# Kernel optimization log

Hardware: AMD Instinct MI355X
Metric: run time of the kernel (lower is better)

Reference implementation:

```python
import jax, jax.numpy as jnp
import numpy as np

B, S, D, H, F, L, V, SPAN = 4, 1024, 1024, 16, 4096, 4, 32000, 512
DH = D // H
NEG = -1e9


def _ln(x, g, b, eps=1e-12):
    m = x.mean(-1, keepdims=True)
    v = ((x - m) ** 2).mean(-1, keepdims=True)
    return (x - m) * jax.lax.rsqrt(v + eps) * g + b


def setup_inputs() -> dict:
    key = jax.random.key(0)
    ks = iter(jax.random.split(key, 40))
    g = lambda shape: jax.random.normal(next(ks), shape, jnp.float32) * 0.02
    inp = {
        "input_ids": jax.random.randint(next(ks), (B, S), 0, V),
        "segment_ids": jnp.zeros((B, S), jnp.int32),
        "attention_mask": jnp.ones((B, S), jnp.float32),
        "tok_emb": g((V, D)),
        "seg_emb": g((2, D)),
        "emb_ln_g": jnp.ones((D,), jnp.float32),
        "emb_ln_b": jnp.zeros((D,), jnp.float32),
        "rel_emb": g((2 * SPAN, D)),
        "Wq": g((L, D, D)), "bq": jnp.zeros((L, D), jnp.float32),
        "Wk": g((L, D, D)), "bk": jnp.zeros((L, D), jnp.float32),
        "Wv": g((L, D, D)), "bv": jnp.zeros((L, D), jnp.float32),
        "Wo": g((L, D, D)), "bo": jnp.zeros((L, D), jnp.float32),
        "ln1_g": jnp.ones((L, D), jnp.float32), "ln1_b": jnp.zeros((L, D), jnp.float32),
        "W1": g((L, D, F)), "b1": jnp.zeros((L, F), jnp.float32),
        "W2": g((L, F, D)), "b2": jnp.zeros((L, D), jnp.float32),
        "ln2_g": jnp.ones((L, D), jnp.float32), "ln2_b": jnp.zeros((L, D), jnp.float32),
    }
    return inp


def _forward(input_ids, segment_ids, attention_mask, tok_emb, seg_emb, emb_ln_g,
             emb_ln_b, rel_emb, Wq, bq, Wk, bk, Wv, bv, Wo, bo, ln1_g, ln1_b,
             W1, b1, W2, b2, ln2_g, ln2_b):
    # BertEmbedding (max_len=0 => no absolute positions): token + segment, LN, mask
    h = _ln(tok_emb[input_ids] + seg_emb[segment_ids], emb_ln_g, emb_ln_b)
    h = h * attention_mask[..., None]

    # relative positions (bucket_size=0 path): rel[q,k] = q - k, clamped into table
    pos = jnp.arange(S)
    rel = pos[:, None] - pos[None, :]                      # [S,S]
    c2p_idx = jnp.clip(rel + SPAN, 0, 2 * SPAN - 1)        # [S,S]
    p2c_idx = jnp.clip(-rel + SPAN, 0, 2 * SPAN - 1)       # [S,S]
    bias = (1.0 - attention_mask)[:, None, None, :] * NEG  # [B,1,1,S] additive mask

    scale = 1.0 / jnp.sqrt(jnp.asarray(DH * 3, h.dtype))   # scale_factor = 1 + |{c2p,p2c}|

    def layer(h, p):
        wq, bq_, wk, bk_, wv, bv_, wo, bo_, g1, b1n, w1, b1f, w2, b2f, g2, b2n = p
        q = (h @ wq + bq_).reshape(B, S, H, DH)
        k = (h @ wk + bk_).reshape(B, S, H, DH)
        v = (h @ wv + bv_).reshape(B, S, H, DH)
        att = jnp.einsum('bqhd,bkhd->bhqk', q, k) * scale
        # disentangled relative-position bias (shared q/k projections on rel table)
        pos_k = (rel_emb @ wk + bk_).reshape(2 * SPAN, H, DH)
        pos_q = (rel_emb @ wq + bq_).reshape(2 * SPAN, H, DH)
        c2p = jnp.einsum('bqhd,phd->bhqp', q, pos_k) * scale   # [B,H,S,2*SPAN]
        att = att + jnp.take_along_axis(c2p, c2p_idx[None, None], axis=-1)
        p2c = jnp.einsum('bkhd,phd->bhkp', k, pos_q) * scale   # [B,H,S,2*SPAN]
        att = att + jnp.swapaxes(
            jnp.take_along_axis(p2c, p2c_idx[None, None], axis=-1), -1, -2)
        probs = jax.nn.softmax(att + bias, axis=-1)
        ctx = jnp.einsum('bhqk,bkhd->bqhd', probs, v).reshape(B, S, D)
        h = _ln(h + ctx @ wo + bo_, g1, b1n)
        ff = jax.nn.gelu(h @ w1 + b1f, approximate=False) @ w2 + b2f
        return _ln(h + ff, g2, b2n), None

    h, _ = jax.lax.scan(layer, h, (Wq, bq, Wk, bk, Wv, bv, Wo, bo,
                                   ln1_g, ln1_b, W1, b1, W2, b2, ln2_g, ln2_b))
    return h


def reference(input_ids, segment_ids, attention_mask, tok_emb, seg_emb, emb_ln_g,
              emb_ln_b, rel_emb, Wq, bq, Wk, bk, Wv, bv, Wo, bo, ln1_g, ln1_b,
              W1, b1, W2, b2, ln2_g, ln2_b):
    return _forward(input_ids, segment_ids, attention_mask, tok_emb, seg_emb,
                    emb_ln_g, emb_ln_b, rel_emb, Wq, bq, Wk, bk, Wv, bv, Wo, bo,
                    ln1_g, ln1_b, W1, b1, W2, b2, ln2_g, ln2_b)
```

## Files before the change

kernel.cpp:

```cpp
#include <hip/hip_runtime.h>

#define DEV __device__ __forceinline__

typedef __bf16 bf16;
typedef __bf16 bf16x4 __attribute__((ext_vector_type(4)));
typedef __bf16 bf16x8 __attribute__((ext_vector_type(8)));
typedef float f32x4 __attribute__((ext_vector_type(4)));

constexpr int B_ = 4, S_ = 1024, D_ = 1024, H_ = 16, F_ = 4096, L_ = 4, SPAN_ = 512, DH_ = 64;
constexpr float SCALE_ = 0.07216878364870322f;
constexpr float LOG2E_ = 1.4426950408889634f;
constexpr float SCL2_ = SCALE_ * LOG2E_;
constexpr float THR2_ = 11.5f;
constexpr long POSL_ = 32L * 1024 * 64;

DEV void gload_lds16(const void* g, void* l) {
  __builtin_amdgcn_global_load_lds((const __attribute__((address_space(1))) void*)g,
                                   (__attribute__((address_space(3))) void*)l, 16, 0, 0);
}

template <int CTRL>
DEV float dppf(float x) {
  return __builtin_bit_cast(
      float, __builtin_amdgcn_mov_dpp(__builtin_bit_cast(int, x), CTRL, 0xf, 0xf, true));
}
DEV float rowMax16(float v) {
  v = fmaxf(v, dppf<0x128>(v));
  v = fmaxf(v, dppf<0x124>(v));
  v = fmaxf(v, dppf<0x122>(v));
  v = fmaxf(v, dppf<0x121>(v));
  return v;
}
DEV float rowSum16(float v) {
  v += dppf<0x128>(v);
  v += dppf<0x124>(v);
  v += dppf<0x122>(v);
  v += dppf<0x121>(v);
  return v;
}

DEV float blockSum4(float v, volatile float* red) {
#pragma unroll
  for (int o = 32; o; o >>= 1) v += __shfl_xor(v, o);
  if ((threadIdx.x & 63) == 0) red[threadIdx.x >> 6] = v;
  __syncthreads();
  return red[0] + red[1] + red[2] + red[3];
}

DEV bf16x8 lds_frag(const bf16* buf, int row, int chunk) {
  return *(const bf16x8*)((const char*)buf + row * 128 + ((chunk ^ (row & 7)) << 4));
}
DEV bf16x8 rdfrag(const char* base, int row, int chunk) {
  return *(const bf16x8*)(base + row * 128 + ((chunk ^ (row & 7)) << 4));
}

template <int EPI>
__global__ __launch_bounds__(512, 1) void gemm256(
    const bf16* __restrict__ A, const bf16* __restrict__ Bm,
    const float* __restrict__ bias, void* __restrict__ Cout,
    int K, int lda, int ldb, int ldc, long sA, long sB, long sC) {
  extern __shared__ __align__(16) char smem[];

  const int z = blockIdx.z;
  A += (long)z * sA;
  Bm += (long)z * sB;
  const long coff = (long)z * sC;

  const int nwg = gridDim.x * gridDim.y;
  const int flat = blockIdx.y * gridDim.x + blockIdx.x;
  const int qq = nwg >> 3;
  const int swz = (flat & 7) * qq + (flat >> 3);
  const int bx = swz % gridDim.x, by = swz / gridDim.x;
  const int m0 = by * 256, n0 = bx * 256;

  const int tid = threadIdx.x, lane = tid & 63, wave = tid >> 6;
  const int wr = wave >> 2, wc = wave & 3;
  const int fr = lane & 15, fq = lane >> 4;

  f32x4 acc[8][4];
#pragma unroll
  for (int m = 0; m < 8; m++)
#pragma unroll
    for (int n = 0; n < 4; n++) acc[m][n] = f32x4{0.f, 0.f, 0.f, 0.f};

  const int r8 = tid >> 3;
  const int swzel = ((tid & 7) ^ (r8 & 7)) << 3;
  const bf16* ga = A + (long)(m0 + r8) * lda + swzel;
  const bf16* gb = Bm + (long)(n0 + r8) * ldb + swzel;

  const int NT = K >> 6;

  auto stage = [&](int t) {
    const long ko = (long)t * 64;
    char* da = smem + ((t & 1) << 15) + wave * 1024;
    gload_lds16(ga + ko, da);
    gload_lds16(ga + 64 * (long)lda + ko, da + 8192);
    gload_lds16(ga + 128 * (long)lda + ko, da + 16384);
    gload_lds16(ga + 192 * (long)lda + ko, da + 24576);
    char* db = smem + 65536 + ((t & 1) << 15) + wave * 1024;
    gload_lds16(gb + ko, db);
    gload_lds16(gb + 64 * (long)ldb + ko, db + 8192);
    gload_lds16(gb + 128 * (long)ldb + ko, db + 16384);
    gload_lds16(gb + 192 * (long)ldb + ko, db + 24576);
  };

  stage(0);
  asm volatile("s_waitcnt vmcnt(0)" ::: "memory");
  __builtin_amdgcn_s_barrier();

  for (int j = 0; j < NT; j++) {
    const char* Ac = smem + ((j & 1) << 15);
    const char* Bc = smem + 65536 + ((j & 1) << 15);

    if (j + 1 < NT) stage(j + 1);

    bf16x8 af[4][2], bfg[4][2];
#pragma unroll
    for (int m = 0; m < 4; m++) {
      const int ar = wr * 128 + m * 16 + fr;
      af[m][0] = rdfrag(Ac, ar, fq);
      af[m][1] = rdfrag(Ac, ar, 4 + fq);
    }
#pragma unroll
    for (int n = 0; n < 4; n++) {
      const int br = wc * 64 + n * 16 + fr;
      bfg[n][0] = rdfrag(Bc, br, fq);
      bfg[n][1] = rdfrag(Bc, br, 4 + fq);
    }

    __builtin_amdgcn_s_setprio(1);
#pragma unroll
    for (int m = 0; m < 4; m++)
#pragma unroll
      for (int n = 0; n < 4; n++)
#pragma unroll
        for (int kc = 0; kc < 2; kc++)
          acc[m][n] = __builtin_amdgcn_mfma_f32_16x16x32_bf16(af[m][kc], bfg[n][kc],
                                                              acc[m][n], 0, 0, 0);
    __builtin_amdgcn_s_setprio(0);
    __builtin_amdgcn_sched_barrier(0);

#pragma unroll
    for (int m = 0; m < 4; m++) {
      const int ar = wr * 128 + (m + 4) * 16 + fr;
      af[m][0] = rdfrag(Ac, ar, fq);
      af[m][1] = rdfrag(Ac, ar, 4 + fq);
    }
    __builtin_amdgcn_s_setprio(1);
#pragma unroll
    for (int m = 0; m < 4; m++)
#pragma unroll
      for (int n = 0; n < 4; n++)
#pragma unroll
        for (int kc = 0; kc < 2; kc++)
          acc[m + 4][n] = __builtin_amdgcn_mfma_f32_16x16x32_bf16(af[m][kc], bfg[n][kc],
                                                                  acc[m + 4][n], 0, 0, 0);
    __builtin_amdgcn_s_setprio(0);

    asm volatile("s_waitcnt vmcnt(0)" ::: "memory");
    __builtin_amdgcn_s_barrier();
  }

#pragma unroll
  for (int m = 0; m < 8; m++) {
#pragma unroll
    for (int n = 0; n < 4; n++) {
      const int col = n0 + wc * 64 + n * 16 + fr;
      float bval = 0.f;
      if constexpr (EPI == 3 || EPI == 4) bval = bias ? bias[col] : 0.f;
#pragma unroll
      for (int rr = 0; rr < 4; rr++) {
        const int row = m0 + wr * 128 + m * 16 + fq * 4 + rr;
        const long idx = coff + (long)row * ldc + col;
        const float v = acc[m][n][rr];
        if constexpr (EPI == 0) ((float*)Cout)[idx] = v;
        else if constexpr (EPI == 3) ((bf16*)Cout)[idx] = (bf16)(v + bval);
        else if constexpr (EPI == 4) {
          float x = v + bval;
          x = 0.5f * x * (1.f + erff(x * 0.70710678118654752f));
          ((bf16*)Cout)[idx] = (bf16)x;
        }
      }
    }
  }
}

template <int EPI>
__global__ __launch_bounds__(256) void gemm_bt(
    const bf16* __restrict__ A, const bf16* __restrict__ Bm,
    const float* __restrict__ bias, void* __restrict__ Cout,
    int M, int N, int K, int lda, int ldb, int ldc, float alpha,
    long sA, long sB, long sC, long sBias) {
  __shared__ alignas(16) bf16 As[128 * 64];
  __shared__ alignas(16) bf16 Bs[128 * 64];

  const int z = blockIdx.z;
  A += (long)z * sA;
  Bm += (long)z * sB;
  bias += (long)z * sBias;
  const long coff = (long)z * sC;

  const int nwg = gridDim.x * gridDim.y;
  const int flat = blockIdx.y * gridDim.x + blockIdx.x;
  const int qq = nwg >> 3;
  const int swz = (flat & 7) * qq + (flat >> 3);
  const int bx = swz % gridDim.x, by = swz / gridDim.x;

  const int m0 = by * 128, n0 = bx * 128;
  const int tid = threadIdx.x, lane = tid & 63, wave = tid >> 6;
  const int wr = wave >> 1, wc = wave & 1;
  const int fr = lane & 15, fq = lane >> 4;

  f32x4 acc[4][4];
#pragma unroll
  for (int m = 0; m < 4; m++)
#pragma unroll
    for (int n = 0; n < 4; n++) acc[m][n] = f32x4{0.f, 0.f, 0.f, 0.f};

  const int r8 = tid >> 3;
  const int swzel = ((tid & 7) ^ (r8 & 7)) << 3;
  const bf16* ga = A + (long)(m0 + r8) * lda + swzel;
  const bf16* gb = Bm + (long)(n0 + r8) * ldb + swzel;
  const int swzrd = fr & 7;

  for (int k0 = 0; k0 < K; k0 += 64) {
#pragma unroll
    for (int i = 0; i < 4; i++)
      gload_lds16(ga + (long)i * 32 * lda + k0, (char*)As + i * 4096 + wave * 1024);
#pragma unroll
    for (int i = 0; i < 4; i++)
      gload_lds16(gb + (long)i * 32 * ldb + k0, (char*)Bs + i * 4096 + wave * 1024);
    __syncthreads();
#pragma unroll
    for (int kc = 0; kc < 2; kc++) {
      bf16x8 af[4], bfv[4];
#pragma unroll
      for (int m = 0; m < 4; m++)
        af[m] = *(const bf16x8*)((char*)As + (wr * 64 + m * 16 + fr) * 128 +
                                 (((kc * 4 + fq) ^ swzrd) << 4));
#pragma unroll
      for (int n = 0; n < 4; n++)
        bfv[n] = *(const bf16x8*)((char*)Bs + (wc * 64 + n * 16 + fr) * 128 +
                                  (((kc * 4 + fq) ^ swzrd) << 4));
#pragma unroll
      for (int m = 0; m < 4; m++)
#pragma unroll
        for (int n = 0; n < 4; n++)
          acc[m][n] = __builtin_amdgcn_mfma_f32_16x16x32_bf16(af[m], bfv[n], acc[m][n], 0, 0, 0);
    }
    __syncthreads();
  }

#pragma unroll
  for (int m = 0; m < 4; m++) {
#pragma unroll
    for (int n = 0; n < 4; n++) {
      const int col = n0 + wc * 64 + n * 16 + fr;
      float bval = 0.f;
      if constexpr (EPI == 3 || EPI == 4 || EPI == 5) bval = bias ? bias[col] : 0.f;
#pragma unroll
      for (int rr = 0; rr < 4; rr++) {
        const int row = m0 + wr * 64 + m * 16 + fq * 4 + rr;
        const long idx = coff + (long)row * ldc + col;
        const float v = acc[m][n][rr];
        if constexpr (EPI == 0) ((float*)Cout)[idx] = v * alpha;
        else if constexpr (EPI == 3) ((bf16*)Cout)[idx] = (bf16)(v + bval);
        else if constexpr (EPI == 4) {
          float x = v + bval;
          x = 0.5f * x * (1.f + erff(x * 0.70710678118654752f));
          ((bf16*)Cout)[idx] = (bf16)x;
        } else if constexpr (EPI == 5) {
          const long pidx = coff + ((long)(col >> 6) * 1024 + row) * 64 + (col & 63);
          ((bf16*)Cout)[pidx] = (bf16)(v + bval);
        }
      }
    }
  }
}

__global__ __launch_bounds__(256) void repack_kv(const bf16* __restrict__ qkv,
                                                 bf16* __restrict__ kp,
                                                 bf16* __restrict__ vp) {
  const int kt = blockIdx.x, bh = blockIdx.y;
  const int b = bh >> 4, h = bh & 15;
  const int k0 = kt * 64;
  __shared__ bf16 t[64][72];
  const int ty = threadIdx.x >> 3, tx = threadIdx.x & 7;
#pragma unroll
  for (int p = 0; p < 2; p++) {
    const int s = k0 + p * 32 + ty;
    const long base = (long)(b * 1024 + s) * 3072 + h * 64;
    bf16x8 kv = *(const bf16x8*)(qkv + base + 1024 + tx * 8);
    *(bf16x8*)(kp + ((long)(bh * 1024 + s) << 6) + tx * 8) = kv;
    bf16x8 vv = *(const bf16x8*)(qkv + base + 2048 + tx * 8);
    *(bf16x8*)(&t[p * 32 + ty][tx * 8]) = vv;
  }
  __syncthreads();
  const int dh = threadIdx.x >> 2, sc = (threadIdx.x & 3) * 16;
  bf16 tmp[16];
#pragma unroll
  for (int j = 0; j < 16; j++) tmp[j] = t[sc + j][dh];
  bf16* dst = vp + ((long)(bh * 16 + kt) << 12) + dh * 64 + sc;
  *(bf16x8*)dst = *(bf16x8*)tmp;
  *(bf16x8*)(dst + 8) = *(bf16x8*)(tmp + 8);
}

__global__ __launch_bounds__(256) void attn_fused(
    const bf16* __restrict__ qkv, const bf16* __restrict__ kp,
    const bf16* __restrict__ vp, const bf16* __restrict__ pospk,
    const float* __restrict__ mask, bf16* __restrict__ ctx) {
  const int id = blockIdx.x;
  const int xcd = id & 7, sub = id >> 3;
  const int bh = xcd + 8 * (sub >> 4);
  const int qt = sub & 15;
  const int b = bh >> 4, h = bh & 15;
  const int q0 = qt * 64;
  const int tid = threadIdx.x, wave = tid >> 6, lane = tid & 63;
  const int fr = lane & 15, fq = lane >> 4;

  __shared__ alignas(16) char smem[79360];
  bf16* PXk = (bf16*)smem;
  char* p_l = smem;
  bf16* PXq = (bf16*)(smem + 16384);
  bf16* Ks = (bf16*)(smem + 32768);
  bf16* Vs = (bf16*)(smem + 40960);
  bf16* c2p_T = (bf16*)(smem + 49152);
  bf16* p2c_T = (bf16*)(smem + 61952);

  const bf16* posq = pospk + ((long)h << 16);
  const bf16* posk = pospk + ((long)(16 + h) << 16);
  const bf16* kbase = kp + ((long)bh << 16);
  const bf16* vbase = vp + ((long)bh << 16);

  bf16x8 qa[2];
  {
    const bf16* qrow = qkv + (long)(b * 1024 + q0 + wave * 16 + fr) * 3072 + h * 64;
    qa[0] = *(const bf16x8*)(qrow + fq * 8);
    qa[1] = *(const bf16x8*)(qrow + 32 + fq * 8);
  }

  f32x4 o[4];
#pragma unroll
  for (int n = 0; n < 4; n++) o[n] = f32x4{0.f, 0.f, 0.f, 0.f};
  float m_r[4], l_r[4];
#pragma unroll
  for (int r = 0; r < 4; r++) { m_r[r] = -1e30f; l_r[r] = 0.f; }

  char* pl_base = p_l + wave * 2048;
  bf16* c2p_w = c2p_T + wave * 1600;
  const int wbyte = wave * 1024;

  for (int kt = 0; kt < 16; kt++) {
    const int k0 = kt * 64;

    __syncthreads();
    {
      const int j0k = q0 - k0 + 449;
      const int j0q = k0 - q0 + 449;
#pragma unroll
      for (int c = 0; c < 4; c++) {
        const int u = c * 256 + tid;
        const int rr = u >> 3;
        const int sel = (((u & 7) ^ (rr & 7)) << 3);
        int jk = j0k + rr;
        jk = jk < 0 ? 0 : (jk > 1023 ? 1023 : jk);
        gload_lds16(posk + ((long)jk << 6) + sel, (char*)PXk + c * 4096 + wbyte);
        int jq = j0q + rr;
        jq = jq < 0 ? 0 : (jq > 1023 ? 1023 : jq);
        gload_lds16(posq + ((long)jq << 6) + sel, (char*)PXq + c * 4096 + wbyte);
      }
#pragma unroll
      for (int c = 0; c < 2; c++) {
        const int u = c * 256 + tid;
        const int rr = u >> 3;
        const int sel = (((u & 7) ^ (rr & 7)) << 3);
        gload_lds16(kbase + ((long)(k0 + rr) << 6) + sel, (char*)Ks + c * 4096 + wbyte);
        gload_lds16(vbase + ((long)kt << 12) + ((long)rr << 6) + sel,
                    (char*)Vs + c * 4096 + wbyte);
      }
    }
    __syncthreads();

    bf16x8 ka[2];
    ka[0] = lds_frag(Ks, wave * 16 + fr, fq);
    ka[1] = lds_frag(Ks, wave * 16 + fr, 4 + fq);
    __builtin_amdgcn_s_setprio(1);
    {
      f32x4 cw[5];
#pragma unroll
      for (int t = 0; t < 5; t++) cw[t] = f32x4{0.f, 0.f, 0.f, 0.f};
#pragma unroll
      for (int kc = 0; kc < 2; kc++)
#pragma unroll
        for (int t = 0; t < 5; t++) {
          const bf16x8 pb = lds_frag(PXk, wave * 16 + t * 16 + fr, kc * 4 + fq);
          cw[t] = __builtin_amdgcn_mfma_f32_16x16x32_bf16(qa[kc], pb, cw[t], 0, 0, 0);
        }
#pragma unroll
      for (int t = 0; t < 5; t++) {
        bf16x4 pk;
#pragma unroll
        for (int r = 0; r < 4; r++) pk[r] = (bf16)cw[t][r];
        *(bf16x4*)&c2p_w[(t * 16 + fr) * 20 + fq * 4] = pk;
      }
    }
    f32x4 s[4];
#pragma unroll
    for (int n = 0; n < 4; n++) s[n] = f32x4{0.f, 0.f, 0.f, 0.f};
#pragma unroll
    for (int kc = 0; kc < 2; kc++)
#pragma unroll
      for (int n = 0; n < 4; n++) {
        const bf16x8 kb = lds_frag(Ks, n * 16 + fr, kc * 4 + fq);
        s[n] = __builtin_amdgcn_mfma_f32_16x16x32_bf16(qa[kc], kb, s[n], 0, 0, 0);
      }
    {
      f32x4 pw[5];
#pragma unroll
      for (int t = 0; t < 5; t++) pw[t] = f32x4{0.f, 0.f, 0.f, 0.f};
#pragma unroll
      for (int kc = 0; kc < 2; kc++)
#pragma unroll
        for (int t = 0; t < 5; t++) {
          const bf16x8 pb = lds_frag(PXq, (wave + t) * 16 + fr, kc * 4 + fq);
          pw[t] = __builtin_amdgcn_mfma_f32_16x16x32_bf16(ka[kc], pb, pw[t], 0, 0, 0);
        }
#pragma unroll
      for (int t = 0; t < 5; t++) {
        bf16x4 pk;
#pragma unroll
        for (int r = 0; r < 4; r++) pk[r] = (bf16)pw[t][r];
        *(bf16x4*)&p2c_T[((wave + t) * 16 + fr) * 68 + wave * 16 + fq * 4] = pk;
      }
    }
    __builtin_amdgcn_s_setprio(0);
    __syncthreads();

    bf16x8 vb[2][4];
#pragma unroll
    for (int kc = 0; kc < 2; kc++)
#pragma unroll
      for (int n = 0; n < 4; n++) vb[kc][n] = lds_frag(Vs, n * 16 + fr, kc * 4 + fq);

    float st[4][4];
#pragma unroll
    for (int n = 0; n < 4; n++) {
      const int ki = n * 16 + fr;
      const float mb = (1.0f - mask[b * S_ + k0 + ki]) * (-1e9f * LOG2E_);
#pragma unroll
      for (int r = 0; r < 4; r++) {
        const int qi_s = fq * 4 + r;
        const float cv = (float)c2p_w[(qi_s - ki + 63) * 20 + qi_s];
        const float pv = (float)p2c_T[(ki - (wave * 16 + qi_s) + 63) * 68 + ki];
        st[n][r] = (s[n][r] + cv + pv) * SCL2_ + mb;
      }
    }

    float pmax[4];
#pragma unroll
    for (int r = 0; r < 4; r++) {
      float v = fmaxf(fmaxf(st[0][r], st[1][r]), fmaxf(st[2][r], st[3][r]));
      pmax[r] = rowMax16(v);
    }
    const bool ok = (pmax[0] - m_r[0] <= THR2_) && (pmax[1] - m_r[1] <= THR2_) &&
                    (pmax[2] - m_r[2] <= THR2_) && (pmax[3] - m_r[3] <= THR2_);
    if (!__all(ok)) {
#pragma unroll
      for (int r = 0; r < 4; r++) {
        const float mn = fmaxf(m_r[r], pmax[r]);
        const float sc = exp2f(m_r[r] - mn);
        m_r[r] = mn;
        l_r[r] *= sc;
#pragma unroll
        for (int n = 0; n < 4; n++) o[n][r] *= sc;
      }
    }
    float rs[4] = {0.f, 0.f, 0.f, 0.f};
#pragma unroll
    for (int n = 0; n < 4; n++) {
      const int ki = n * 16 + fr;
#pragma unroll
      for (int r = 0; r < 4; r++) {
        const int qi_s = fq * 4 + r;
        const float p = exp2f(st[n][r] - m_r[r]);
        rs[r] += p;
        *(bf16*)(pl_base + qi_s * 128 + ((ki * 2) ^ ((qi_s & 7) << 4))) = (bf16)p;
      }
    }
#pragma unroll
    for (int r = 0; r < 4; r++) l_r[r] += rowSum16(rs[r]);

#pragma unroll
    for (int kc = 0; kc < 2; kc++) {
      const bf16x8 pa =
          *(const bf16x8*)(pl_base + fr * 128 + ((kc * 64 + fq * 16) ^ ((fr & 7) << 4)));
#pragma unroll
      for (int n = 0; n < 4; n++)
        o[n] = __builtin_amdgcn_mfma_f32_16x16x32_bf16(pa, vb[kc][n], o[n], 0, 0, 0);
    }
  }

#pragma unroll
  for (int r = 0; r < 4; r++) {
    const float inv = 1.f / l_r[r];
    const long row = (long)(b * S_ + q0 + wave * 16 + fq * 4 + r) * D_ + h * 64;
#pragma unroll
    for (int n = 0; n < 4; n++) ctx[row + n * 16 + fr] = (bf16)(o[n][r] * inv);
  }
}

__global__ __launch_bounds__(256) void wtrans4(const float* __restrict__ Wq,
                                               const float* __restrict__ Wk,
                                               const float* __restrict__ Wv,
                                               const float* __restrict__ Wo,
                                               bf16* __restrict__ wqkvT,
                                               bf16* __restrict__ woT) {
  const int z = blockIdx.z;
  const int l = z >> 2, which = z & 3;
  const long DD = (long)D_ * D_;
  const float* W = (which == 0 ? Wq : which == 1 ? Wk : which == 2 ? Wv : Wo) + l * DD;
  bf16* WT = (which < 3) ? (wqkvT + (long)l * 3 * DD + which * DD) : (woT + (long)l * DD);
  __shared__ float t[32][33];
  const int n0 = blockIdx.x * 32, k0 = blockIdx.y * 32;
  const int tx = threadIdx.x & 31, ty = threadIdx.x >> 5;
#pragma unroll
  for (int i = ty; i < 32; i += 8) t[i][tx] = W[(long)(k0 + i) * D_ + n0 + tx];
  __syncthreads();
#pragma unroll
  for (int i = ty; i < 32; i += 8) WT[(long)(n0 + i) * D_ + k0 + tx] = (bf16)t[tx][i];
}

__global__ __launch_bounds__(256) void wtrans(const float* __restrict__ W,
                                              bf16* __restrict__ WT, int K, int N,
                                              long sW, long sT) {
  W += (long)blockIdx.z * sW;
  WT += (long)blockIdx.z * sT;
  __shared__ float t[32][33];
  const int n0 = blockIdx.x * 32, k0 = blockIdx.y * 32;
  const int tx = threadIdx.x & 31, ty = threadIdx.x >> 5;
#pragma unroll
  for (int i = ty; i < 32; i += 8) t[i][tx] = W[(long)(k0 + i) * N + n0 + tx];
  __syncthreads();
#pragma unroll
  for (int i = ty; i < 32; i += 8) WT[(long)(n0 + i) * K + k0 + tx] = (bf16)t[tx][i];
}

__global__ __launch_bounds__(256) void f2b(const float* __restrict__ in,
                                           bf16* __restrict__ out, long n) {
  long i = (long)blockIdx.x * 256 + threadIdx.x;
  if (i < n) out[i] = (bf16)in[i];
}

__global__ __launch_bounds__(256) void bias_concat(const float* __restrict__ bq,
                                                   const float* __restrict__ bk,
                                                   const float* __restrict__ bv,
                                                   float* __restrict__ bqkv) {
  const int i = blockIdx.x * 256 + threadIdx.x;
  const int l = i / (3 * D_), s = (i % (3 * D_)) / D_, d = i % D_;
  const float* src = s == 0 ? bq : (s == 1 ? bk : bv);
  bqkv[i] = src[l * D_ + d];
}

__global__ __launch_bounds__(256) void embed_ln(
    const int* __restrict__ ids, const int* __restrict__ segs,
    const float* __restrict__ mask, const float* __restrict__ tok,
    const float* __restrict__ seg, const float* __restrict__ g,
    const float* __restrict__ bta, float* __restrict__ h, bf16* __restrict__ hb) {
  __shared__ float r1[4], r2[4];
  const int t = blockIdx.x;
  const int d4 = threadIdx.x;
  const long tb4 = (long)ids[t] * 256;
  const long sb4 = (long)segs[t] * 256;
  const long b4 = (long)t * 256;
  f32x4 x = ((const f32x4*)tok)[tb4 + d4];
  const f32x4 sv = ((const f32x4*)seg)[sb4 + d4];
#pragma unroll
  for (int r = 0; r < 4; r++) x[r] += sv[r];
  float sm = x[0] + x[1] + x[2] + x[3];
  sm = blockSum4(sm, r1);
  const float mean = sm * (1.f / D_);
  float vs = 0.f;
#pragma unroll
  for (int r = 0; r < 4; r++) {
    const float c = x[r] - mean;
    vs += c * c;
  }
  vs = blockSum4(vs, r2);
  const float rstd = rsqrtf(vs * (1.f / D_) + 1e-12f);
  const float mk = mask[t];
  const f32x4 gv = ((const f32x4*)g)[d4];
  const f32x4 bv = ((const f32x4*)bta)[d4];
  f32x4 y;
  bf16x4 yb;
#pragma unroll
  for (int r = 0; r < 4; r++) {
    y[r] = ((x[r] - mean) * rstd * gv[r] + bv[r]) * mk;
    yb[r] = (bf16)y[r];
  }
  ((f32x4*)h)[b4 + d4] = y;
  *(bf16x4*)&hb[(b4 + d4) * 4] = yb;
}

template <int P>
__global__ __launch_bounds__(256) void ln_residual_red(
    const float* __restrict__ hin, float* __restrict__ hout,
    const float* __restrict__ part, long pstride4,
    const float* __restrict__ bias, const float* __restrict__ g,
    const float* __restrict__ bta, bf16* __restrict__ hb) {
  __shared__ float r1[4], r2[4];
  const int d4 = threadIdx.x;
  const long b4 = (long)blockIdx.x * 256;
  f32x4 x = ((const f32x4*)hin)[b4 + d4];
  const f32x4 bi = ((const f32x4*)bias)[d4];
#pragma unroll
  for (int r = 0; r < 4; r++) x[r] += bi[r];
#pragma unroll
  for (int z = 0; z < P; z++) {
    const f32x4 pv = ((const f32x4*)part)[(long)z * pstride4 + b4 + d4];
#pragma unroll
    for (int r = 0; r < 4; r++) x[r] += pv[r];
  }
  float sm = x[0] + x[1] + x[2] + x[3];
  sm = blockSum4(sm, r1);
  const float mean = sm * (1.f / D_);
  float vs = 0.f;
#pragma unroll
  for (int r = 0; r < 4; r++) {
    const float c = x[r] - mean;
    vs += c * c;
  }
  vs = blockSum4(vs, r2);
  const float rstd = rsqrtf(vs * (1.f / D_) + 1e-12f);
  const f32x4 gv = ((const f32x4*)g)[d4];
  const f32x4 bv = ((const f32x4*)bta)[d4];
  f32x4 y;
  bf16x4 yb;
#pragma unroll
  for (int r = 0; r < 4; r++) {
    y[r] = (x[r] - mean) * rstd * gv[r] + bv[r];
    yb[r] = (bf16)y[r];
  }
  ((f32x4*)hout)[b4 + d4] = y;
  *(bf16x4*)&hb[(b4 + d4) * 4] = yb;
}

extern "C" void kernel_launch(void* const* d_in, const int* in_sizes, int n_in,
                              void* d_out, int out_size, void* d_ws, size_t ws_size,
                              hipStream_t stream) {
  (void)in_sizes; (void)n_in; (void)out_size; (void)ws_size;
  const int* input_ids = (const int*)d_in[0];
  const int* segment_ids = (const int*)d_in[1];
  const float* attention_mask = (const float*)d_in[2];
  const float* tok_emb = (const float*)d_in[3];
  const float* seg_emb = (const float*)d_in[4];
  const float* emb_ln_g = (const float*)d_in[5];
  const float* emb_ln_b = (const float*)d_in[6];
  const float* rel_emb = (const float*)d_in[7];
  const float* Wq = (const float*)d_in[8];
  const float* bq = (const float*)d_in[9];
  const float* Wk = (const float*)d_in[10];
  const float* bk = (const float*)d_in[11];
  const float* Wv = (const float*)d_in[12];
  const float* bv = (const float*)d_in[13];
  const float* Wo = (const float*)d_in[14];
  const float* bo = (const float*)d_in[15];
  const float* ln1_g = (const float*)d_in[16];
  const float* ln1_b = (const float*)d_in[17];
  const float* W1 = (const float*)d_in[18];
  const float* b1 = (const float*)d_in[19];
  const float* W2 = (const float*)d_in[20];
  const float* b2 = (const float*)d_in[21];
  const float* ln2_g = (const float*)d_in[22];
  const float* ln2_b = (const float*)d_in[23];

  const long DD = (long)D_ * D_;
  const long DF = (long)D_ * F_;
  const int D3 = 3 * D_;

  char* ws = (char*)d_ws;
  auto alloc = [&](size_t bytes) {
    char* p = ws;
    ws += (bytes + 255) & ~(size_t)255;
    return p;
  };
  bf16* wqkvT = (bf16*)alloc((size_t)L_ * 3 * DD * 2);
  bf16* woT = (bf16*)alloc((size_t)L_ * DD * 2);
  bf16* w1T = (bf16*)alloc((size_t)L_ * DF * 2);
  bf16* w2T = (bf16*)alloc((size_t)L_ * DF * 2);
  float* bqkv = (float*)alloc((size_t)L_ * 3 * D_ * 4);
  bf16* relb = (bf16*)alloc((size_t)2 * SPAN_ * D_ * 2);
  float* hbuf = (float*)alloc((size_t)B_ * S_ * D_ * 4);
  bf16* hb = (bf16*)alloc((size_t)B_ * S_ * D_ * 2);
  bf16* qkv = (bf16*)alloc((size_t)B_ * S_ * 3 * D_ * 2);
  bf16* kp = (bf16*)alloc((size_t)B_ * H_ * S_ * DH_ * 2);
  bf16* vp = (bf16*)alloc((size_t)B_ * H_ * S_ * DH_ * 2);
  bf16* pospk = (bf16*)alloc((size_t)L_ * POSL_ * 2);
  bf16* ctxb = (bf16*)alloc((size_t)B_ * S_ * D_ * 2);
  bf16* ff1b = (bf16*)alloc((size_t)B_ * S_ * F_ * 2);
  float* kpart = (float*)alloc((size_t)4 * B_ * S_ * D_ * 4);
  const long PSTR = (long)B_ * S_ * D_;

  wtrans4<<<dim3(D_ / 32, D_ / 32, 4 * L_), 256, 0, stream>>>(Wq, Wk, Wv, Wo, wqkvT, woT);
  wtrans<<<dim3(F_ / 32, D_ / 32, L_), 256, 0, stream>>>(W1, w1T, D_, F_, DF, DF);
  wtrans<<<dim3(D_ / 32, F_ / 32, L_), 256, 0, stream>>>(W2, w2T, F_, D_, DF, DF);
  bias_concat<<<dim3(L_ * 3 * D_ / 256), 256, 0, stream>>>(bq, bk, bv, bqkv);
  f2b<<<dim3((2 * SPAN_ * D_) / 256), 256, 0, stream>>>(rel_emb, relb, (long)2 * SPAN_ * D_);
  gemm_bt<5><<<dim3((2 * D_) / 128, (2 * SPAN_) / 128, L_), 256, 0, stream>>>(
      relb, wqkvT, bqkv, pospk, 2 * SPAN_, 2 * D_, D_, D_, D_, 0, 1.f,
      0, 3 * DD, POSL_, 3 * D_);
  embed_ln<<<dim3(B_ * S_), 256, 0, stream>>>(input_ids, segment_ids, attention_mask,
                                              tok_emb, seg_emb, emb_ln_g, emb_ln_b, hbuf, hb);

  const size_t SH = 131072;

  for (int l = 0; l < L_; ++l) {
    const bf16* wqkv_ = wqkvT + (long)l * 3 * DD;
    const bf16* wo_ = woT + (long)l * DD;
    const bf16* w1_ = w1T + (long)l * DF;
    const bf16* w2_ = w2T + (long)l * DF;
    const float* bqkv_ = bqkv + (long)l * 3 * D_;
    const float* bo_ = bo + (long)l * D_;
    const float* b1_ = b1 + (long)l * F_;
    const float* b2_ = b2 + (long)l * D_;

    gemm_bt<3><<<dim3(D3 / 128, (B_ * S_) / 128, 1), 256, 0, stream>>>(
        hb, wqkv_, bqkv_, qkv, B_ * S_, D3, D_, D_, D_, D3, 1.f, 0, 0, 0, 0);
    repack_kv<<<dim3(16, B_ * H_), 256, 0, stream>>>(qkv, kp, vp);

    attn_fused<<<dim3(1024), 256, 0, stream>>>(qkv, kp, vp, pospk + (long)l * POSL_,
                                               attention_mask, ctxb);

    gemm_bt<0><<<dim3(D_ / 128, (B_ * S_) / 128, 2), 256, 0, stream>>>(
        ctxb, wo_, nullptr, kpart, B_ * S_, D_, D_ / 2, D_, D_, D_, 1.f,
        D_ / 2, D_ / 2, PSTR, 0);
    ln_residual_red<2><<<dim3(B_ * S_), 256, 0, stream>>>(
        hbuf, hbuf, kpart, PSTR / 4, bo_, ln1_g + l * D_, ln1_b + l * D_, hb);

    gemm256<4><<<dim3(F_ / 256, (B_ * S_) / 256, 1), 512, SH, stream>>>(
        hb, w1_, b1_, ff1b, D_, D_, D_, F_, 0, 0, 0);
    gemm256<0><<<dim3(D_ / 256, (B_ * S_) / 256, 4), 512, SH, stream>>>(
        ff1b, w2_, nullptr, kpart, F_ / 4, F_, F_, D_, F_ / 4, F_ / 4, PSTR);
    float* hout = (l == L_ - 1) ? (float*)d_out : hbuf;
    ln_residual_red<4><<<dim3(B_ * S_), 256, 0, stream>>>(
        hbuf, hout, kpart, PSTR / 4, b2_, ln2_g + l * D_, ln2_b + l * D_, hb);
  }
}
```

Before: 1.308 ms.

## Share one LDS buffer for pos-key and pos-query tiles to cut shared memory

Aliases the PXk and PXq position-embedding tiles into a single LDS buffer. The posq tile is loaded after the c2p and QK MFMAs finish, behind two extra block barriers. The p2c scatter is changed to a diagonal-packed layout that stores only the needed entries, with a bounds check, and reads are indexed accordingly. Shared memory drops from about 79 KB to 54 KB so more blocks can be resident per CU. The cost is an extra serialized global-to-LDS load phase and two more __syncthreads per key tile.

```diff
diff --git a/kernel.cpp b/kernel.cpp
--- a/kernel.cpp
+++ b/kernel.cpp
@@ -318,14 +318,13 @@
   const int tid = threadIdx.x, wave = tid >> 6, lane = tid & 63;
   const int fr = lane & 15, fq = lane >> 4;
 
-  __shared__ alignas(16) char smem[79360];
-  bf16* PXk = (bf16*)smem;
+  __shared__ alignas(16) char smem[54272];
+  bf16* PX = (bf16*)smem;
   char* p_l = smem;
-  bf16* PXq = (bf16*)(smem + 16384);
-  bf16* Ks = (bf16*)(smem + 32768);
-  bf16* Vs = (bf16*)(smem + 40960);
-  bf16* c2p_T = (bf16*)(smem + 49152);
-  bf16* p2c_T = (bf16*)(smem + 61952);
+  bf16* Ks = (bf16*)(smem + 16384);
+  bf16* Vs = (bf16*)(smem + 24576);
+  bf16* c2p_T = (bf16*)(smem + 32768);
+  bf16* p2c_P = (bf16*)(smem + 45568);
 
   const bf16* posq = pospk + ((long)h << 16);
   const bf16* posk = pospk + ((long)(16 + h) << 16);
@@ -356,7 +355,6 @@
     __syncthreads();
     {
       const int j0k = q0 - k0 + 449;
-      const int j0q = k0 - q0 + 449;
 #pragma unroll
       for (int c = 0; c < 4; c++) {
         const int u = c * 256 + tid;
@@ -364,10 +362,7 @@
         const int sel = (((u & 7) ^ (rr & 7)) << 3);
         int jk = j0k + rr;
         jk = jk < 0 ? 0 : (jk > 1023 ? 1023 : jk);
-        gload_lds16(posk + ((long)jk << 6) + sel, (char*)PXk + c * 4096 + wbyte);
-        int jq = j0q + rr;
-        jq = jq < 0 ? 0 : (jq > 1023 ? 1023 : jq);
-        gload_lds16(posq + ((long)jq << 6) + sel, (char*)PXq + c * 4096 + wbyte);
+        gload_lds16(posk + ((long)jk << 6) + sel, (char*)PX + c * 4096 + wbyte);
       }
 #pragma unroll
       for (int c = 0; c < 2; c++) {
@@ -393,7 +388,7 @@
       for (int kc = 0; kc < 2; kc++)
 #pragma unroll
         for (int t = 0; t < 5; t++) {
-          const bf16x8 pb = lds_frag(PXk, wave * 16 + t * 16 + fr, kc * 4 + fq);
+          const bf16x8 pb = lds_frag(PX, wave * 16 + t * 16 + fr, kc * 4 + fq);
           cw[t] = __builtin_amdgcn_mfma_f32_16x16x32_bf16(qa[kc], pb, cw[t], 0, 0, 0);
         }
 #pragma unroll
@@ -414,6 +409,24 @@
         const bf16x8 kb = lds_frag(Ks, n * 16 + fr, kc * 4 + fq);
         s[n] = __builtin_amdgcn_mfma_f32_16x16x32_bf16(qa[kc], kb, s[n], 0, 0, 0);
       }
+    __builtin_amdgcn_s_setprio(0);
+    __syncthreads();
+
+    {
+      const int j0q = k0 - q0 + 449;
+#pragma unroll
+      for (int c = 0; c < 4; c++) {
+        const int u = c * 256 + tid;
+        const int rr = u >> 3;
+        const int sel = (((u & 7) ^ (rr & 7)) << 3);
+        int jq = j0q + rr;
+        jq = jq < 0 ? 0 : (jq > 1023 ? 1023 : jq);
+        gload_lds16(posq + ((long)jq << 6) + sel, (char*)PX + c * 4096 + wbyte);
+      }
+    }
+    __syncthreads();
+
+    __builtin_amdgcn_s_setprio(1);
     {
       f32x4 pw[5];
 #pragma unroll
@@ -422,15 +435,17 @@
       for (int kc = 0; kc < 2; kc++)
 #pragma unroll
         for (int t = 0; t < 5; t++) {
-          const bf16x8 pb = lds_frag(PXq, (wave + t) * 16 + fr, kc * 4 + fq);
+          const bf16x8 pb = lds_frag(PX, (wave + t) * 16 + fr, kc * 4 + fq);
           pw[t] = __builtin_amdgcn_mfma_f32_16x16x32_bf16(ka[kc], pb, pw[t], 0, 0, 0);
         }
 #pragma unroll
       for (int t = 0; t < 5; t++) {
-        bf16x4 pk;
-#pragma unroll
-        for (int r = 0; r < 4; r++) pk[r] = (bf16)pw[t][r];
-        *(bf16x4*)&p2c_T[((wave + t) * 16 + fr) * 68 + wave * 16 + fq * 4] = pk;
+#pragma unroll
+        for (int r = 0; r < 4; r++) {
+          const int toff = t * 16 + fr - fq * 4 - r;
+          if ((unsigned)toff < 64u)
+            p2c_P[(wave * 16 + fq * 4 + r) * 68 + toff] = (bf16)pw[t][r];
+        }
       }
     }
     __builtin_amdgcn_s_setprio(0);
@@ -451,7 +466,7 @@
       for (int r = 0; r < 4; r++) {
         const int qi_s = fq * 4 + r;
         const float cv = (float)c2p_w[(qi_s - ki + 63) * 20 + qi_s];
-        const float pv = (float)p2c_T[(ki - (wave * 16 + qi_s) + 63) * 68 + ki];
+        const float pv = (float)p2c_P[ki * 68 + (63 - (wave * 16 + qi_s))];
         st[n][r] = (s[n][r] + cv + pv) * SCL2_ + mb;
       }
     }
```

After: 1.330 ms. About the same (+1.7%).
